# Kernel tuning notes

Measured on AMD Instinct MI355X. Metric: run time of the kernel, lower is better.

## Reference

```python
import jax, jax.numpy as jnp
import numpy as np

B, V, D, P = 32, 21, 512, 64
IN, OUT = D * P, 720
E, K, R, H = 8, 2, 16, 256
SCALING = 16.0 / R  # lora alpha / rank = 1.0
TEMP = 1.0


def setup_inputs() -> dict:
    key = jax.random.key(0)
    ks = jax.random.split(key, 9)
    s = lambda k, shape, fan: jax.random.normal(k, shape, dtype=jnp.float32) * (1.0 / np.sqrt(fan))
    return {
        "x": jax.random.normal(ks[0], (B, V, D, P), dtype=jnp.float32),
        "W_base": s(ks[1], (OUT, IN), IN),
        "b_base": s(ks[2], (OUT,), IN),
        "W_r1": s(ks[3], (H, D), D),
        "b_r1": s(ks[4], (H,), D),
        "W_r2": s(ks[5], (E, H), H),
        "b_r2": s(ks[6], (E,), H),
        "lora_A": s(ks[7], (E, R, IN), IN),
        "lora_B": s(ks[8], (E, OUT, R), R),
    }


def reference(x, W_base, b_base, W_r1, b_r1, W_r2, b_r2, lora_A, lora_B):
    # base head: flatten last two dims -> linear (dropout is identity in eval)
    flattened = x.reshape(B, V, IN)                      # [B, V, D*P]
    base_out = flattened @ W_base.T + b_base             # [B, V, OUT]

    # learned router on pooled features (dropout identity, no noise in eval)
    pooled = x.mean(axis=(1, 3))                         # [B, D]
    h = jax.nn.gelu(pooled @ W_r1.T + b_r1, approximate=False)
    logits = h @ W_r2.T + b_r2                           # [B, E]
    probs = jax.nn.softmax(logits / TEMP, axis=-1)
    topk_w, topk_idx = jax.lax.top_k(probs, K)           # [B, K]
    topk_w = topk_w / jnp.clip(topk_w.sum(-1, keepdims=True), 1e-6)

    # all LoRA experts on all samples (matches original), then gather top-k
    flat2d = flattened.reshape(B * V, IN)
    low = jnp.einsum('ni,eri->enr', flat2d, lora_A)      # [E, BV, R]
    delta = jnp.einsum('enr,eor->eno', low, lora_B) * SCALING  # [E, BV, OUT]
    stack = delta.reshape(E, B, V, OUT).transpose(1, 0, 2, 3)  # [B, E, V, OUT]
    sel = jnp.take_along_axis(stack, topk_idx[:, :, None, None], axis=1)  # [B, K, V, OUT]
    moe_delta = (topk_w[:, :, None, None] * sel).sum(axis=1)  # [B, V, OUT]

    return base_out + moe_delta, probs
```

## Files before the change

### kernel.cpp

```cpp
#include <hip/hip_runtime.h>
#include <math.h>

constexpr int Bz = 32, Vz = 21, Dz = 512, Pz = 64;
constexpr int INz = Dz * Pz;
constexpr int OUTz = 720;
constexpr int Ez = 8, Rz = 16, Hz = 256;
constexpr int Mz = Bz * Vz;
constexpr int Nz = OUTz + Ez * Rz;
constexpr int Kz = INz;

constexpr int BM = 128, BN = 128, BK = 32;
constexpr int SPLIT = 16;
constexpr int KSL = Kz / SPLIT;
constexpr int NCH = KSL / BK;
constexpr int LDA = 36;

typedef _Float16 f16x8 __attribute__((ext_vector_type(8)));
typedef __fp16  fp16x2 __attribute__((ext_vector_type(2)));
typedef float f32x4 __attribute__((ext_vector_type(4)));

__device__ __forceinline__ unsigned int cvt2(float a, float b) {
    fp16x2 p = __builtin_amdgcn_cvt_pkrtz(a, b);
    return __builtin_bit_cast(unsigned int, p);
}

__device__ __forceinline__ void barrier_lgkm() {
    asm volatile("s_waitcnt lgkmcnt(0)\n\ts_barrier" ::: "memory");
}

template <bool PART>
__global__ __launch_bounds__(256, 3)
void gemm_pool_kernel(const float* __restrict__ x, const float* __restrict__ Wb,
                      const float* __restrict__ lA, float* __restrict__ part,
                      float* __restrict__ C, float* __restrict__ pooled)
{
    __shared__ _Float16 As[2][BM * LDA];
    __shared__ _Float16 Bs[2][BN * LDA];
    __shared__ float plocal[BM][NCH / 2];

    const int id = blockIdx.x;
    const int x8 = id & 7;
    const int k8 = id >> 3;
    const int nt = k8 % 7;
    const int mt = (k8 / 7) % 6;
    const int s  = (k8 / 42) * 8 + x8;

    const int t  = threadIdx.x;
    const int r  = t >> 1;
    const int h  = t & 1;
    const int kbase = s * KSL + h * 16;

    int gm = mt * BM + r;
    const bool mval = (gm < Mz);
    if (!mval) gm = Mz - 1;
    const float* pa = x + (size_t)gm * Kz + kbase;

    int gn = nt * BN + r;
    if (gn >= Nz) gn = Nz - 1;
    const float* pb = (gn < OUTz) ? (Wb + (size_t)gn * Kz + kbase)
                                  : (lA + (size_t)(gn - OUTz) * Kz + kbase);

    const int wave = t >> 6, lane = t & 63;
    const int wr = (wave >> 1) * 64;
    const int wc = (wave & 1) * 64;
    const int fl = lane & 15;
    const int ko = (lane >> 4) * 8;

    f32x4 acc[4][4] = {};

    float4 ca[2][4], cb[2][4];
    #pragma unroll
    for (int q = 0; q < 4; ++q) {
        ca[0][q] = *(const float4*)(pa + 4 * q);
        cb[0][q] = *(const float4*)(pb + 4 * q);
        ca[1][q] = *(const float4*)(pa + BK + 4 * q);
        cb[1][q] = *(const float4*)(pb + BK + 4 * q);
    }

    const bool do_pool = (nt == 0) && mval;
    float psum = 0.0f;

#define GSTEP(SET, CIDX)                                                          \
    {                                                                             \
        const int c_ = (CIDX);                                                    \
        if (do_pool) {                                                            \
            psum += (ca[SET][0].x + ca[SET][0].y + ca[SET][0].z + ca[SET][0].w)   \
                  + (ca[SET][1].x + ca[SET][1].y + ca[SET][1].z + ca[SET][1].w)   \
                  + (ca[SET][2].x + ca[SET][2].y + ca[SET][2].z + ca[SET][2].w)   \
                  + (ca[SET][3].x + ca[SET][3].y + ca[SET][3].z + ca[SET][3].w);  \
        }                                                                         \
        if (SET == 1) {           \
            float ps2 = psum + __shfl_down(psum, 1, 64);                          \
            if (do_pool && h == 0) plocal[r][c_ >> 1] = ps2;                      \
            psum = 0.0f;                                                          \
        }                                                                         \
        _Float16* wA = &As[SET][r * LDA + h * 16];                                \
        *((uint4*)wA)     = make_uint4(                                           \
            cvt2(ca[SET][0].x, ca[SET][0].y), cvt2(ca[SET][0].z, ca[SET][0].w),   \
            cvt2(ca[SET][1].x, ca[SET][1].y), cvt2(ca[SET][1].z, ca[SET][1].w));  \
        *((uint4*)wA + 1) = make_uint4(                                           \
            cvt2(ca[SET][2].x, ca[SET][2].y), cvt2(ca[SET][2].z, ca[SET][2].w),   \
            cvt2(ca[SET][3].x, ca[SET][3].y), cvt2(ca[SET][3].z, ca[SET][3].w));  \
        _Float16* wB = &Bs[SET][r * LDA + h * 16];                                \
        *((uint4*)wB)     = make_uint4(                                           \
            cvt2(cb[SET][0].x, cb[SET][0].y), cvt2(cb[SET][0].z, cb[SET][0].w),   \
            cvt2(cb[SET][1].x, cb[SET][1].y), cvt2(cb[SET][1].z, cb[SET][1].w));  \
        *((uint4*)wB + 1) = make_uint4(                                           \
            cvt2(cb[SET][2].x, cb[SET][2].y), cvt2(cb[SET][2].z, cb[SET][2].w),   \
            cvt2(cb[SET][3].x, cb[SET][3].y), cvt2(cb[SET][3].z, cb[SET][3].w));  \
        if (c_ + 2 < NCH) {                                                       \
            const float* qa = pa + (c_ + 2) * BK;                                 \
            const float* qb = pb + (c_ + 2) * BK;                                 \
            _Pragma("unroll")                                                     \
            for (int q = 0; q < 4; ++q) {                                         \
                ca[SET][q] = *(const float4*)(qa + 4 * q);                        \
                cb[SET][q] = *(const float4*)(qb + 4 * q);                        \
            }                                                                     \
        }                                                                         \
        barrier_lgkm();                                                           \
        f16x8 af[4], bfr[4];                                                      \
        _Pragma("unroll")                                                         \
        for (int i = 0; i < 4; ++i)                                               \
            af[i] = *(const f16x8*)(&As[SET][(wr + i * 16 + fl) * LDA + ko]);     \
        _Pragma("unroll")                                                         \
        for (int j = 0; j < 4; ++j)                                               \
            bfr[j] = *(const f16x8*)(&Bs[SET][(wc + j * 16 + fl) * LDA + ko]);    \
        _Pragma("unroll")                                                         \
        for (int i = 0; i < 4; ++i)                                               \
            _Pragma("unroll")                                                     \
            for (int j = 0; j < 4; ++j)                                           \
                acc[i][j] = __builtin_amdgcn_mfma_f32_16x16x32_f16(               \
                                af[i], bfr[j], acc[i][j], 0, 0, 0);               \
    }

    for (int cc = 0; cc < NCH; cc += 2) {
        GSTEP(0, cc)
        GSTEP(1, cc + 1)
    }
#undef GSTEP

    if (nt == 0) {
        __syncthreads();
        for (int idx = t; idx < BM * (NCH / 2); idx += 256) {
            const int rr = idx / (NCH / 2), j = idx % (NCH / 2);
            const int g = mt * BM + rr;
            if (g < Mz) atomicAdd(&pooled[(g / Vz) * Dz + s * (NCH / 2) + j], plocal[rr][j]);
        }
    }

    const int rq = (lane >> 4) * 4;
    float* dst = PART ? (part + (size_t)s * Mz * Nz) : C;
    #pragma unroll
    for (int i = 0; i < 4; ++i) {
        const int gmr0 = mt * BM + wr + i * 16 + rq;
        #pragma unroll
        for (int j = 0; j < 4; ++j) {
            const int gnc = nt * BN + wc + j * 16 + fl;
            if (gnc < Nz) {
                #pragma unroll
                for (int q2 = 0; q2 < 4; ++q2) {
                    const int gmr = gmr0 + q2;
                    if (gmr < Mz) {
                        if (PART) dst[(size_t)gmr * Nz + gnc] = acc[i][j][q2];
                        else      atomicAdd(&dst[(size_t)gmr * Nz + gnc], acc[i][j][q2]);
                    }
                }
            }
        }
    }
}

__global__ __launch_bounds__(256)
void router_kernel(const float* __restrict__ pooled_raw,
                   const float* __restrict__ Wr1, const float* __restrict__ br1,
                   const float* __restrict__ Wr2, const float* __restrict__ br2,
                   float* __restrict__ probs_out, int* __restrict__ tki, float* __restrict__ tkw)
{
    const int b = blockIdx.x, t = threadIdx.x;
    const int wave = t >> 6, lane = t & 63;
    __shared__ float hbuf[Hz];
    __shared__ float lg[Ez];

    const float sc = 1.0f / (float)(Vz * Pz);
    float pv[8];
    const float* prow = pooled_raw + b * Dz + lane * 8;
    #pragma unroll
    for (int u = 0; u < 8; ++u) pv[u] = prow[u] * sc;

    for (int i0 = 0; i0 < 64; i0 += 4) {
        float v[4];
        #pragma unroll
        for (int u = 0; u < 4; ++u) {
            const int j = wave * 64 + i0 + u;
            const float* wrow = Wr1 + (size_t)j * Dz + lane * 8;
            float4 w0 = *(const float4*)(wrow);
            float4 w1 = *(const float4*)(wrow + 4);
            v[u] = pv[0]*w0.x + pv[1]*w0.y + pv[2]*w0.z + pv[3]*w0.w
                 + pv[4]*w1.x + pv[5]*w1.y + pv[6]*w1.z + pv[7]*w1.w;
        }
        #pragma unroll
        for (int u = 0; u < 4; ++u) {
            #pragma unroll
            for (int off = 32; off >= 1; off >>= 1) v[u] += __shfl_down(v[u], off, 64);
        }
        if (lane == 0) {
            #pragma unroll
            for (int u = 0; u < 4; ++u) {
                const int j = wave * 64 + i0 + u;
                float a = v[u] + br1[j];
                hbuf[j] = 0.5f * a * (1.0f + erff(a * 0.70710678118654752440f));
            }
        }
    }
    __syncthreads();

    if (t < Ez) {
        const float* w = Wr2 + (size_t)t * Hz;
        float a = br2[t];
        for (int j = 0; j < Hz; ++j) a = fmaf(hbuf[j], w[j], a);
        lg[t] = a;
    }
    __syncthreads();

    if (t == 0) {
        float mx = lg[0];
        for (int e = 1; e < Ez; ++e) mx = fmaxf(mx, lg[e]);
        float p[Ez], ssum = 0.0f;
        for (int e = 0; e < Ez; ++e) { p[e] = expf(lg[e] - mx); ssum += p[e]; }
        const float inv = 1.0f / ssum;
        for (int e = 0; e < Ez; ++e) { p[e] *= inv; probs_out[b * Ez + e] = p[e]; }
        int i0 = 0;
        for (int e = 1; e < Ez; ++e) if (p[e] > p[i0]) i0 = e;
        int i1 = (i0 == 0) ? 1 : 0;
        for (int e = 0; e < Ez; ++e) if (e != i0 && p[e] > p[i1]) i1 = e;
        float s2 = p[i0] + p[i1];
        if (s2 < 1e-6f) s2 = 1e-6f;
        tki[b * 2] = i0; tki[b * 2 + 1] = i1;
        tkw[b * 2] = p[i0] / s2; tkw[b * 2 + 1] = p[i1] / s2;
    }
}

template <bool PART>
__global__ __launch_bounds__(256)
void combine_kernel(const float* __restrict__ part, const float* __restrict__ C,
                    const float* __restrict__ bb, const float* __restrict__ loraB,
                    const int* __restrict__ tki, const float* __restrict__ tkw,
                    float* __restrict__ out)
{
    const int m = blockIdx.x;
    const int t = threadIdx.x;
    const int b = m / Vz;
    const int e0 = tki[b * 2], e1 = tki[b * 2 + 1];
    const float w0 = tkw[b * 2], w1 = tkw[b * 2 + 1];

    __shared__ float lw[2 * Rz];
    if (t < 2 * Rz) {
        const int e = (t < Rz) ? e0 : e1;
        const size_t off = (size_t)m * Nz + OUTz + e * Rz + (t & (Rz - 1));
        float v = 0.0f;
        if (PART) {
            #pragma unroll
            for (int ss = 0; ss < SPLIT; ++ss) v += part[(size_t)ss * Mz * Nz + off];
        } else v = C[off];
        lw[t] = v;
    }
    __syncthreads();

    for (int o = t; o < OUTz; o += 256) {
        float acc = bb[o];
        if (PART) {
            #pragma unroll
            for (int ss = 0; ss < SPLIT; ++ss)
                acc += part[(size_t)ss * Mz * Nz + (size_t)m * Nz + o];
        } else acc += C[(size_t)m * Nz + o];
        const float* B0 = loraB + ((size_t)e0 * OUTz + o) * Rz;
        const float* B1 = loraB + ((size_t)e1 * OUTz + o) * Rz;
        float d0 = 0.0f, d1 = 0.0f;
        #pragma unroll
        for (int rr = 0; rr < Rz; ++rr) {
            d0 = fmaf(lw[rr], B0[rr], d0);
            d1 = fmaf(lw[Rz + rr], B1[rr], d1);
        }
        out[(size_t)m * OUTz + o] = acc + w0 * d0 + w1 * d1;
    }
}

extern "C" void kernel_launch(void* const* d_in, const int* in_sizes, int n_in,
                              void* d_out, int out_size, void* d_ws, size_t ws_size,
                              hipStream_t stream)
{
    const float* x   = (const float*)d_in[0];
    const float* Wb  = (const float*)d_in[1];
    const float* bb  = (const float*)d_in[2];
    const float* Wr1 = (const float*)d_in[3];
    const float* br1 = (const float*)d_in[4];
    const float* Wr2 = (const float*)d_in[5];
    const float* br2 = (const float*)d_in[6];
    const float* lA  = (const float*)d_in[7];
    const float* lB  = (const float*)d_in[8];
    float* out = (float*)d_out;

    const size_t part_elems = (size_t)SPLIT * Mz * Nz;
    const size_t need = (part_elems + Bz * Dz + 256) * sizeof(float);
    const bool use_part = (ws_size >= need);

    if (use_part) {
        float* part   = (float*)d_ws;
        float* pooled = part + part_elems;
        int*   tki    = (int*)(pooled + Bz * Dz);
        float* tkw    = (float*)(tki + 2 * Bz);

        (void)hipMemsetAsync(pooled, 0, Bz * Dz * sizeof(float), stream);

        gemm_pool_kernel<true><<<dim3(7 * 6 * SPLIT), 256, 0, stream>>>(
            x, Wb, lA, part, nullptr, pooled);
        router_kernel<<<Bz, 256, 0, stream>>>(pooled, Wr1, br1, Wr2, br2,
                                              out + (size_t)Mz * OUTz, tki, tkw);
        combine_kernel<true><<<Mz, 256, 0, stream>>>(part, nullptr, bb, lB, tki, tkw, out);
    } else {
        float* C      = (float*)d_ws;
        float* pooled = C + (size_t)Mz * Nz;
        int*   tki    = (int*)(pooled + Bz * Dz);
        float* tkw    = (float*)(tki + 2 * Bz);

        (void)hipMemsetAsync(d_ws, 0, ((size_t)Mz * Nz + Bz * Dz) * sizeof(float), stream);

        gemm_pool_kernel<false><<<dim3(7 * 6 * SPLIT), 256, 0, stream>>>(
            x, Wb, lA, nullptr, C, pooled);
        router_kernel<<<Bz, 256, 0, stream>>>(pooled, Wr1, br1, Wr2, br2,
                                              out + (size_t)Mz * OUTz, tki, tkw);
        combine_kernel<false><<<Mz, 256, 0, stream>>>(nullptr, C, bb, lB, tki, tkw, out);
    }
}
```

Baseline: 363.0 us.

## Pre-convert inputs to fp16 and use async LDS-load GEMM with larger tiles

Adds a conversion pass that turns x and the weight matrices into fp16 buffers and computes the pooled sums with atomics. A new GEMM kernel uses global_load_lds direct-to-LDS copies with triple buffering, 256x128 tiles, 512 threads and split-K of 32. This is meant to take conversion and register staging off the GEMM's critical path. In exchange it adds extra memory traffic for writing and rereading the fp16 copies, a larger partial-sum buffer for combine to reduce, and a much bigger workspace requirement.

Result: faster. 349.8 us (-3.6%).

```diff
diff --git a/kernel.cpp b/kernel.cpp
--- a/kernel.cpp
+++ b/kernel.cpp
@@ -15,6 +15,14 @@
 constexpr int NCH = KSL / BK;
 constexpr int LDA = 36;
 
+constexpr int BM2 = 256, BN2 = 128, BK2 = 32;
+constexpr int SPLIT2 = 32;
+constexpr int KSL2 = Kz / SPLIT2;
+constexpr int NCH2 = KSL2 / BK2;
+constexpr int ABUF = BM2 * BK2;
+constexpr int BBUF = BN2 * BK2;
+constexpr int SLOT = ABUF + BBUF;
+
 typedef _Float16 f16x8 __attribute__((ext_vector_type(8)));
 typedef __fp16  fp16x2 __attribute__((ext_vector_type(2)));
 typedef float f32x4 __attribute__((ext_vector_type(4)));
@@ -26,6 +34,12 @@
 
 __device__ __forceinline__ void barrier_lgkm() {
     asm volatile("s_waitcnt lgkmcnt(0)\n\ts_barrier" ::: "memory");
+}
+
+__device__ __forceinline__ void gload16(const _Float16* g, _Float16* l) {
+    __builtin_amdgcn_global_load_lds(
+        (const __attribute__((address_space(1))) unsigned int*)g,
+        (__attribute__((address_space(3))) unsigned int*)l, 16, 0, 0);
 }
 
 template <bool PART>
@@ -89,7 +103,7 @@
                   + (ca[SET][2].x + ca[SET][2].y + ca[SET][2].z + ca[SET][2].w)   \
                   + (ca[SET][3].x + ca[SET][3].y + ca[SET][3].z + ca[SET][3].w);  \
         }                                                                         \
-        if (SET == 1) {           \
+        if (SET == 1) {                                                           \
             float ps2 = psum + __shfl_down(psum, 1, 64);                          \
             if (do_pool && h == 0) plocal[r][c_ >> 1] = ps2;                      \
             psum = 0.0f;                                                          \
@@ -171,6 +185,134 @@
 }
 
 __global__ __launch_bounds__(256)
+void convert_kernel(const float* __restrict__ x, const float* __restrict__ Wb,
+                    const float* __restrict__ lA,
+                    _Float16* __restrict__ xh, _Float16* __restrict__ wh,
+                    float* __restrict__ pooled)
+{
+    const int bid = blockIdx.x, t = threadIdx.x;
+    if (bid < Mz) {
+        const int m = bid, b = m / Vz;
+        const float* src = x + (size_t)m * Kz;
+        _Float16* dst = xh + (size_t)m * Kz;
+        #pragma unroll 4
+        for (int i = 0; i < 16; ++i) {
+            const int i8 = i * 256 + t;
+            const float4 u = *(const float4*)(src + i8 * 8);
+            const float4 v = *(const float4*)(src + i8 * 8 + 4);
+            *(uint4*)(dst + i8 * 8) = make_uint4(cvt2(u.x, u.y), cvt2(u.z, u.w),
+                                                 cvt2(v.x, v.y), cvt2(v.z, v.w));
+            float ssum = (u.x + u.y + u.z + u.w) + (v.x + v.y + v.z + v.w);
+            ssum += __shfl_xor(ssum, 1, 64);
+            ssum += __shfl_xor(ssum, 2, 64);
+            ssum += __shfl_xor(ssum, 4, 64);
+            if ((t & 7) == 0)
+                atomicAdd(&pooled[b * Dz + i * 32 + (t >> 3)], ssum);
+        }
+    } else {
+        const int rr = bid - Mz;
+        const float* src = (rr < OUTz) ? (Wb + (size_t)rr * Kz)
+                                       : (lA + (size_t)(rr - OUTz) * Kz);
+        _Float16* dst = wh + (size_t)rr * Kz;
+        #pragma unroll 4
+        for (int i = 0; i < 16; ++i) {
+            const int i8 = i * 256 + t;
+            const float4 u = *(const float4*)(src + i8 * 8);
+            const float4 v = *(const float4*)(src + i8 * 8 + 4);
+            *(uint4*)(dst + i8 * 8) = make_uint4(cvt2(u.x, u.y), cvt2(u.z, u.w),
+                                                 cvt2(v.x, v.y), cvt2(v.z, v.w));
+        }
+    }
+}
+
+__global__ __launch_bounds__(512, 4)
+void gemm_f16_kernel(const _Float16* __restrict__ xh, const _Float16* __restrict__ wh,
+                     float* __restrict__ part)
+{
+    __shared__ _Float16 sm[3 * SLOT];
+
+    const int id = blockIdx.x;
+    const int x8 = id & 7;
+    const int k8 = id >> 3;
+    const int nt = k8 % 7;
+    const int mt = (k8 / 7) % 3;
+    const int s  = (k8 / 21) * 8 + x8;
+
+    const int t = threadIdx.x;
+    const int wave = t >> 6, lane = t & 63;
+    const int rl = lane >> 2, cc = lane & 3;
+
+    const size_t kb = (size_t)s * KSL2;
+
+    const int rA0 = (wave)     * 16 + rl;
+    const int rA1 = (8 + wave) * 16 + rl;
+    const int rB  = wave * 16 + rl;
+    const _Float16* gA0 = xh + (size_t)min(mt * BM2 + rA0, Mz - 1) * Kz + kb + cc * 8;
+    const _Float16* gA1 = xh + (size_t)min(mt * BM2 + rA1, Mz - 1) * Kz + kb + cc * 8;
+    const _Float16* gB  = wh + (size_t)min(nt * BN2 + rB,  Nz - 1) * Kz + kb + cc * 8;
+
+#define STAGE(SLOTI, CHK)                                                \
+    {                                                                    \
+        _Float16* sA = sm + (SLOTI) * SLOT;                              \
+        _Float16* sB = sA + ABUF;                                        \
+        const size_t ko_ = (size_t)(CHK) * BK2;                          \
+        gload16(gA0 + ko_, sA + wave * 512);                             \
+        gload16(gA1 + ko_, sA + (8 + wave) * 512);                       \
+        gload16(gB  + ko_, sB + wave * 512);                             \
+    }
+
+    STAGE(0, 0)
+    STAGE(1, 1)
+
+    const int wr = (wave >> 1) * 64;
+    const int wc = (wave & 1) * 64;
+    const int fl = lane & 15;
+    const int g8 = (lane >> 4) * 8;
+
+    f32x4 acc[4][4] = {};
+
+    for (int c = 0; c < NCH2; ++c) {
+        if (c + 1 < NCH2) asm volatile("s_waitcnt vmcnt(3) lgkmcnt(0)\n\ts_barrier" ::: "memory");
+        else              asm volatile("s_waitcnt vmcnt(0) lgkmcnt(0)\n\ts_barrier" ::: "memory");
+        if (c + 2 < NCH2) STAGE((c + 2) % 3, c + 2)
+
+        const _Float16* A  = sm + (c % 3) * SLOT;
+        const _Float16* Bp = A + ABUF;
+        f16x8 af[4], bfr[4];
+        #pragma unroll
+        for (int i = 0; i < 4; ++i)
+            af[i] = *(const f16x8*)(A + (wr + i * 16 + fl) * BK2 + g8);
+        #pragma unroll
+        for (int j = 0; j < 4; ++j)
+            bfr[j] = *(const f16x8*)(Bp + (wc + j * 16 + fl) * BK2 + g8);
+        #pragma unroll
+        for (int i = 0; i < 4; ++i)
+            #pragma unroll
+            for (int j = 0; j < 4; ++j)
+                acc[i][j] = __builtin_amdgcn_mfma_f32_16x16x32_f16(af[i], bfr[j], acc[i][j], 0, 0, 0);
+    }
+#undef STAGE
+
+    const int rq = (lane >> 4) * 4;
+    float* dst = part + (size_t)s * Mz * Nz;
+    #pragma unroll
+    for (int i = 0; i < 4; ++i) {
+        const int gmr0 = mt * BM2 + wr + i * 16 + rq;
+        #pragma unroll
+        for (int j = 0; j < 4; ++j) {
+            const int gnc = nt * BN2 + wc + j * 16 + fl;
+            if (gnc < Nz) {
+                #pragma unroll
+                for (int q2 = 0; q2 < 4; ++q2) {
+                    const int gmr = gmr0 + q2;
+                    if (gmr < Mz) dst[(size_t)gmr * Nz + gnc] = acc[i][j][q2];
+                }
+            }
+        }
+    }
+}
+
+__global__ __launch_bounds__(256)
 void router_kernel(const float* __restrict__ pooled_raw,
                    const float* __restrict__ Wr1, const float* __restrict__ br1,
                    const float* __restrict__ Wr2, const float* __restrict__ br2,
@@ -240,7 +382,7 @@
     }
 }
 
-template <bool PART>
+template <bool PART, int SPL>
 __global__ __launch_bounds__(256)
 void combine_kernel(const float* __restrict__ part, const float* __restrict__ C,
                     const float* __restrict__ bb, const float* __restrict__ loraB,
@@ -260,7 +402,7 @@
         float v = 0.0f;
         if (PART) {
             #pragma unroll
-            for (int ss = 0; ss < SPLIT; ++ss) v += part[(size_t)ss * Mz * Nz + off];
+            for (int ss = 0; ss < SPL; ++ss) v += part[(size_t)ss * Mz * Nz + off];
         } else v = C[off];
         lw[t] = v;
     }
@@ -270,7 +412,7 @@
         float acc = bb[o];
         if (PART) {
             #pragma unroll
-            for (int ss = 0; ss < SPLIT; ++ss)
+            for (int ss = 0; ss < SPL; ++ss)
                 acc += part[(size_t)ss * Mz * Nz + (size_t)m * Nz + o];
         } else acc += C[(size_t)m * Nz + o];
         const float* B0 = loraB + ((size_t)e0 * OUTz + o) * Rz;
@@ -300,11 +442,32 @@
     const float* lB  = (const float*)d_in[8];
     float* out = (float*)d_out;
 
+    const size_t part2_elems = (size_t)SPLIT2 * Mz * Nz;
+    const size_t xh_halves   = (size_t)Mz * Kz;
+    const size_t wh_halves   = (size_t)Nz * Kz;
+    const size_t need_fast = part2_elems * sizeof(float)
+                           + (xh_halves + wh_halves) * sizeof(_Float16)
+                           + (size_t)(Bz * Dz) * sizeof(float) + 1024;
+
     const size_t part_elems = (size_t)SPLIT * Mz * Nz;
-    const size_t need = (part_elems + Bz * Dz + 256) * sizeof(float);
-    const bool use_part = (ws_size >= need);
-
-    if (use_part) {
+    const size_t need_old = (part_elems + Bz * Dz + 256) * sizeof(float);
+
+    if (ws_size >= need_fast) {
+        float*    part   = (float*)d_ws;
+        _Float16* xh     = (_Float16*)(part + part2_elems);
+        _Float16* wh     = xh + xh_halves;
+        float*    pooled = (float*)(wh + wh_halves);
+        int*      tki    = (int*)(pooled + Bz * Dz);
+        float*    tkw    = (float*)(tki + 2 * Bz);
+
+        (void)hipMemsetAsync(pooled, 0, Bz * Dz * sizeof(float), stream);
+
+        convert_kernel<<<Mz + Nz, 256, 0, stream>>>(x, Wb, lA, xh, wh, pooled);
+        gemm_f16_kernel<<<3 * 7 * SPLIT2, 512, 0, stream>>>(xh, wh, part);
+        router_kernel<<<Bz, 256, 0, stream>>>(pooled, Wr1, br1, Wr2, br2,
+                                              out + (size_t)Mz * OUTz, tki, tkw);
+        combine_kernel<true, SPLIT2><<<Mz, 256, 0, stream>>>(part, nullptr, bb, lB, tki, tkw, out);
+    } else if (ws_size >= need_old) {
         float* part   = (float*)d_ws;
         float* pooled = part + part_elems;
         int*   tki    = (int*)(pooled + Bz * Dz);
@@ -316,7 +479,7 @@
             x, Wb, lA, part, nullptr, pooled);
         router_kernel<<<Bz, 256, 0, stream>>>(pooled, Wr1, br1, Wr2, br2,
                                               out + (size_t)Mz * OUTz, tki, tkw);
-        combine_kernel<true><<<Mz, 256, 0, stream>>>(part, nullptr, bb, lB, tki, tkw, out);
+        combine_kernel<true, SPLIT><<<Mz, 256, 0, stream>>>(part, nullptr, bb, lB, tki, tkw, out);
     } else {
         float* C      = (float*)d_ws;
         float* pooled = C + (size_t)Mz * Nz;
@@ -329,6 +492,6 @@
             x, Wb, lA, nullptr, C, pooled);
         router_kernel<<<Bz, 256, 0, stream>>>(pooled, Wr1, br1, Wr2, br2,
                                               out + (size_t)Mz * OUTz, tki, tkw);
-        combine_kernel<false><<<Mz, 256, 0, stream>>>(nullptr, C, bb, lB, tki, tkw, out);
-    }
-}
+        combine_kernel<false, SPLIT><<<Mz, 256, 0, stream>>>(nullptr, C, bb, lB, tki, tkw, out);
+    }
+}
```
